# Kernel tuning notes

Measured on AMD Instinct MI355X. Metric: run time of the kernel, lower is better.

The kernel has to match this reference:

```python
import jax, jax.numpy as jnp
from jax import lax
import numpy as np

EPS = 1e-5

def _conv1x1(x, w, b=None):
    # x: [B,C,H,W], w: [O,C]
    y = jnp.einsum('oc,bchw->bohw', w, x)
    if b is not None:
        y = y + b[:, None, None]
    return y

def _bn(x, g, b, m, v):
    scale = g / jnp.sqrt(v + EPS)
    return (x - m[:, None, None]) * scale[:, None, None] + b[:, None, None]

def _conv_bn_silu(x, w, g, b, m, v):
    return jax.nn.silu(_bn(_conv1x1(x, w), g, b, m, v))

def _maxpool(x, k):
    p = k // 2
    return lax.reduce_window(x, -jnp.inf, lax.max, (1, 1, k, k), (1, 1, 1, 1),
                             ((0, 0), (0, 0), (p, p), (p, p)))

def _avgpool(x, k):
    # torch AvgPool2d default count_include_pad=True -> divide by k*k
    p = k // 2
    s = lax.reduce_window(x, 0.0, lax.add, (1, 1, k, k), (1, 1, 1, 1),
                          ((0, 0), (0, 0), (p, p), (p, p)))
    return s / float(k * k)

def setup_inputs() -> dict:
    key = jax.random.key(0)
    ks = jax.random.split(key, 18)
    f32 = jnp.float32
    B, C1, H, W = 8, 512, 64, 64
    c_ = C1 // 2          # 256
    C = c_ * 7            # 1792
    Cq = C // 8           # 224
    C2 = 512
    rn = lambda i, sh, s: jax.random.normal(ks[i], sh, dtype=f32) * s
    return {
        'x': rn(0, (B, C1, H, W), 1.0),
        'cv1_w': rn(1, (c_, C1), 0.05),
        'cv1_g': jax.random.uniform(ks[2], (c_,), dtype=f32),
        'cv1_b': rn(3, (c_,), 0.05),
        'cv1_m': jnp.zeros((c_,), f32),
        'cv1_v': jnp.ones((c_,), f32),
        'q_w': rn(4, (Cq, C), 0.02),
        'q_b': rn(5, (Cq,), 0.02),
        'k_w': rn(6, (Cq, C), 0.02),
        'k_b': rn(7, (Cq,), 0.02),
        'v_w': rn(8, (C, C), 0.02),
        'v_b': rn(9, (C,), 0.02),
        'gamma': rn(10, (1,), 0.5),
        'cv2_w': rn(11, (C2, C), 0.02),
        'cv2_g': jax.random.uniform(ks[12], (C2,), dtype=f32),
        'cv2_b': rn(13, (C2,), 0.05),
        'cv2_m': jnp.zeros((C2,), f32),
        'cv2_v': jnp.ones((C2,), f32),
    }

def _criss_cross(cat, q_w, q_b, k_w, k_b, v_w, v_b, gamma):
    B, C, H, W = cat.shape
    q = _conv1x1(cat, q_w, q_b)   # [B,Cq,H,W]
    k = _conv1x1(cat, k_w, k_b)
    v = _conv1x1(cat, v_w, v_b)   # [B,C,H,W]
    # column (H-axis) energies with -inf diagonal, row (W-axis) energies
    eH = jnp.einsum('bchw,bcgw->bhwg', q, k)        # [B,H,W,H]
    diag = jnp.eye(H, dtype=bool)[:, None, :]       # mask where h == g
    eH = jnp.where(diag, -jnp.inf, eH)
    eW = jnp.einsum('bchw,bchv->bhwv', q, k)        # [B,H,W,W]
    att = jax.nn.softmax(jnp.concatenate([eH, eW], axis=-1), axis=-1)
    attH, attW = att[..., :H], att[..., H:]
    outH = jnp.einsum('bcgw,bhwg->bchw', v, attH)
    outW = jnp.einsum('bchv,bhwv->bchw', v, attW)
    return gamma[0] * (outH + outW) + cat

def reference(x, cv1_w, cv1_g, cv1_b, cv1_m, cv1_v,
              q_w, q_b, k_w, k_b, v_w, v_b, gamma,
              cv2_w, cv2_g, cv2_b, cv2_m, cv2_v):
    x1 = _conv_bn_silu(x, cv1_w, cv1_g, cv1_b, cv1_m, cv1_v)   # [B,256,H,W]
    y1 = _maxpool(x1, 5)
    y2 = _maxpool(y1, 5)
    y3 = _maxpool(y2, 5)
    a1 = _avgpool(x1, 13)
    a2 = _avgpool(x1, 9)
    a3 = _avgpool(x1, 5)
    cat = jnp.concatenate([x1, y1, y2, y3, a1, a2, a3], axis=1)  # [B,1792,H,W]
    att = _criss_cross(cat, q_w, q_b, k_w, k_b, v_w, v_b, gamma)
    return _conv_bn_silu(att, cv2_w, cv2_g, cv2_b, cv2_m, cv2_v)
```

## Files before the change

kernel.cpp:

```cpp
#include <hip/hip_runtime.h>


typedef short bf16x8 __attribute__((ext_vector_type(8)));
typedef float f32x4  __attribute__((ext_vector_type(4)));

#define DEV __device__ __forceinline__

DEV float bf2f(unsigned short u) {
    unsigned int i = ((unsigned int)u) << 16;
    float f; __builtin_memcpy(&f, &i, 4); return f;
}
DEV unsigned short f2bf(float f) {
    unsigned int i; __builtin_memcpy(&i, &f, 4);
    unsigned int r = i + 0x7FFFu + ((i >> 16) & 1u);
    return (unsigned short)(r >> 16);
}
DEV float fsilu(float v) { return v / (1.f + __expf(-v)); }

#define GLL(gsrc, ldst)                                                        \
    __builtin_amdgcn_global_load_lds(                                          \
        (const __attribute__((address_space(1))) unsigned int*)(gsrc),         \
        (__attribute__((address_space(3))) unsigned int*)(ldst), 16, 0, 0)

#define MFMA(a, b, c) __builtin_amdgcn_mfma_f32_16x16x32_bf16((a), (b), (c), 0, 0, 0)

#define SBAR do {                                                              \
    __builtin_amdgcn_sched_barrier(0);                                         \
    __builtin_amdgcn_s_barrier();                                              \
    __builtin_amdgcn_sched_barrier(0); } while (0)
#define LGKM0 do {                                                             \
    asm volatile("s_waitcnt lgkmcnt(0)" ::: "memory");                         \
    __builtin_amdgcn_sched_barrier(0); } while (0)
#define VMC(n) do {                                                            \
    asm volatile("s_waitcnt vmcnt(" #n ")" ::: "memory");                      \
    __builtin_amdgcn_sched_barrier(0); } while (0)

template <int EPI, bool DUAL>
DEV void gemm_core(
    unsigned short (&Ash)[2][2][8192], unsigned short (&Bsh)[2][2][8192],
    int bx, int by,
    const unsigned short* __restrict__ A, const unsigned short* __restrict__ B,
    const unsigned short* __restrict__ A2, const unsigned short* __restrict__ B2,
    int lda, int ldb, int K1, int K2,
    void* __restrict__ outp, int ldo,
    const float* __restrict__ p0, const float* __restrict__ p1)
{
    const int tid = threadIdx.x, lane = tid & 63, wave = tid >> 6;
    const int wm = wave >> 2, wn = wave & 3;
    const long tile_m = (long)bx * 256;
    const long tile_n = (long)by * 256;
    const int r0 = tid >> 2;
    const int ke0 = ((tid & 3) * 8) ^ (16 * ((r0 >> 3) & 1));
    const unsigned short* As0 = A + (tile_m + r0) * (long)lda + ke0;
    const unsigned short* As1 = A + (tile_m + r0 + 128) * (long)lda + ke0;
    const unsigned short* Bs0 = B + (tile_n + r0) * (long)ldb + ke0;
    const unsigned short* Bs1 = B + (tile_n + r0 + 128) * (long)ldb + ke0;
    const unsigned short* Cs0 = DUAL ? A2 + (tile_m + r0) * (long)lda + ke0 : As0;
    const unsigned short* Cs1 = DUAL ? A2 + (tile_m + r0 + 128) * (long)lda + ke0 : As1;
    const unsigned short* Ds0 = DUAL ? B2 + (tile_n + r0) * (long)ldb + ke0 : Bs0;
    const unsigned short* Ds1 = DUAL ? B2 + (tile_n + r0 + 128) * (long)ldb + ke0 : Bs1;
    const int dst0 = wave * 512;
    const int dst1 = 4096 + wave * 512;
    const int arow = lane & 15;
    const int kgs = ((lane >> 4) << 3) ^ (16 * ((arow >> 3) & 1));
    f32x4 acc[8][4] = {};
    bf16x8 a[8], b[4];
    const int nt1 = K1 >> 6;
    const int nt = nt1 + (DUAL ? (K2 >> 6) : 0);

#define PA0(t) ((DUAL && (t) >= nt1) ? Cs0 + (long)((t) - nt1) * 64 : As0 + (long)(t) * 64)
#define PA1(t) ((DUAL && (t) >= nt1) ? Cs1 + (long)((t) - nt1) * 64 : As1 + (long)(t) * 64)
#define PB0(t) ((DUAL && (t) >= nt1) ? Ds0 + (long)((t) - nt1) * 64 : Bs0 + (long)(t) * 64)
#define PB1(t) ((DUAL && (t) >= nt1) ? Ds1 + (long)((t) - nt1) * 64 : Bs1 + (long)(t) * 64)
#define STGA(db, kh, t) do {                                                   \
    GLL(PA0(t) + (kh) * 32, &Ash[db][kh][dst0]);                               \
    GLL(PA1(t) + (kh) * 32, &Ash[db][kh][dst1]); } while (0)
#define STGB(db, kh, t) do {                                                   \
    GLL(PB0(t) + (kh) * 32, &Bsh[db][kh][dst0]);                               \
    GLL(PB1(t) + (kh) * 32, &Bsh[db][kh][dst1]); } while (0)
#define LDA8(db, ks) do { _Pragma("unroll")                                    \
    for (int m = 0; m < 8; ++m)                                                \
        a[m] = *(const bf16x8*)&Ash[db][ks][(wm * 128 + m * 16 + arow) * 32 + kgs]; \
    } while (0)
#define LDB1(db, ks, n, slot)                                                  \
    b[slot] = *(const bf16x8*)&Bsh[db][ks][(wn * 64 + (n) * 16 + arow) * 32 + kgs]
#define MMA2(lo) do {                                                          \
    __builtin_amdgcn_s_setprio(1);                                             \
    _Pragma("unroll")                                                          \
    for (int m = 0; m < 8; ++m) {                                              \
        acc[m][lo]     = MFMA(a[m], b[lo],     acc[m][lo]);                    \
        acc[m][lo + 1] = MFMA(a[m], b[lo + 1], acc[m][lo + 1]);                \
    }                                                                          \
    __builtin_amdgcn_s_setprio(0); } while (0)

    STGA(0, 0, 0); STGB(0, 0, 0);
    STGA(0, 1, 0); STGB(0, 1, 0);
    {
        const int t1p = (1 < nt) ? 1 : 0;
        STGA(1, 0, t1p); STGB(1, 0, t1p);
    }
    VMC(4);
    SBAR;

    for (int kt = 0; kt < nt; ++kt) {
        const int db = kt & 1, sb = db ^ 1;
        const int t1c = (kt + 1 < nt) ? kt + 1 : nt - 1;
        const int t2c = (kt + 2 < nt) ? kt + 2 : nt - 1;
        LDA8(db, 0);
        LDB1(db, 0, 0, 0); LDB1(db, 0, 1, 1);
        STGA(sb, 1, t1c);
        LGKM0;
        MMA2(0);
        SBAR;
        LDB1(db, 0, 2, 2); LDB1(db, 0, 3, 3);
        STGB(sb, 1, t1c);
        LGKM0;
        MMA2(2);
        SBAR;
        LDA8(db, 1);
        LDB1(db, 1, 0, 0); LDB1(db, 1, 1, 1);
        STGA(db, 0, t2c);
        LGKM0;
        MMA2(0);
        SBAR;
        LDB1(db, 1, 2, 2); LDB1(db, 1, 3, 3);
        STGB(db, 0, t2c);
        LGKM0;
        MMA2(2);
        VMC(4);
        SBAR;
    }
    VMC(0);

    const int rbase = (lane >> 4) << 2;
#pragma unroll
    for (int n = 0; n < 4; ++n) {
        const int gcol = (int)tile_n + wn * 64 + n * 16 + arow;
        const float s0 = p0[gcol];
        const float s1 = (EPI != 1) ? p1[gcol] : 0.f;
#pragma unroll
        for (int m = 0; m < 8; ++m) {
            const long grow0 = tile_m + wm * 128 + m * 16 + rbase;
            if (EPI == 4) {
                const long bb = grow0 >> 12, pix = grow0 & 4095;
                float4 o4;
#pragma unroll
                for (int r = 0; r < 4; ++r) {
                    float v = acc[m][n][r] * s0 + s1;
                    ((float*)&o4)[r] = fsilu(v);
                }
                *(float4*)&((float*)outp)[((bb * 512 + gcol)) * 4096 + pix] = o4;
            } else {
#pragma unroll
                for (int r = 0; r < 4; ++r) {
                    float v = acc[m][n][r];
                    if (EPI != 1) { v = v * s0 + s1; v = fsilu(v); }
                    else          { v += s0; }
                    ((unsigned short*)outp)[(grow0 + r) * ldo + gcol] = f2bf(v);
                }
            }
        }
    }
#undef PA0
#undef PA1
#undef PB0
#undef PB1
#undef STGA
#undef STGB
#undef LDA8
#undef LDB1
#undef MMA2
}

template <int EPI, bool DUAL>
__global__ __launch_bounds__(512, 2) void gemm_pair(
    const unsigned short* __restrict__ A, const unsigned short* __restrict__ B,
    const unsigned short* __restrict__ A2, const unsigned short* __restrict__ B2,
    int lda, int ldb, int K1, int K2,
    void* __restrict__ outp, int ldo,
    const float* __restrict__ p0, const float* __restrict__ p1)
{
    __shared__ __align__(16) unsigned short Ash[2][2][8192];
    __shared__ __align__(16) unsigned short Bsh[2][2][8192];
    const int bid = blockIdx.x;
    const int xcd = bid & 7, idx = bid >> 3;
    const int m = xcd + 8 * (idx >> 1);
    const int n = idx & 1;
    gemm_core<EPI, DUAL>(Ash, Bsh, m, n, A, B, A2, B2, lda, ldb, K1, K2,
                         outp, ldo, p0, p1);
}

__global__ __launch_bounds__(512, 2) void gemm_wcv1(
    const unsigned short* __restrict__ wc2, const unsigned short* __restrict__ wvT,
    unsigned short* __restrict__ w2g, const float* __restrict__ zeros,
    const unsigned short* __restrict__ xT, const unsigned short* __restrict__ wb1,
    unsigned short* __restrict__ catT,
    const float* __restrict__ sc1, const float* __restrict__ sh1)
{
    __shared__ __align__(16) unsigned short Ash[2][2][8192];
    __shared__ __align__(16) unsigned short Bsh[2][2][8192];
    const int bid = blockIdx.x;
    if (bid < 14) {
        const int bx = bid / 7, by = bid % 7;
        gemm_core<1, false>(Ash, Bsh, bx, by, wc2, wvT, wc2, wvT,
                            1792, 1792, 1792, 0, w2g, 1792, zeros, nullptr);
    } else {
        const int bx = bid - 14;
        gemm_core<0, false>(Ash, Bsh, bx, 0, xT, wb1, xT, wb1,
                            512, 512, 512, 0, catT, 1792, sc1, sh1);
    }
}

__global__ __launch_bounds__(256) void prep_all(
    const float* __restrict__ x, unsigned short* __restrict__ xT,
    const float* __restrict__ v_w, unsigned short* __restrict__ wvT,
    const float* __restrict__ cv1_w, const float* __restrict__ cv1_g,
    const float* __restrict__ cv1_b, const float* __restrict__ cv1_m,
    const float* __restrict__ cv1_v,
    const float* __restrict__ q_w, const float* __restrict__ q_b,
    const float* __restrict__ k_w, const float* __restrict__ k_b,
    const float* __restrict__ cv2_w,
    unsigned short* __restrict__ wb1, unsigned short* __restrict__ wqk,
    unsigned short* __restrict__ wc2,
    float* __restrict__ sc1, float* __restrict__ sh1,
    float* __restrict__ qkb, float* __restrict__ zeros,
    const float* __restrict__ cv2_g, const float* __restrict__ cv2_b,
    const float* __restrict__ cv2_m, const float* __restrict__ cv2_v,
    const float* __restrict__ v_b, const float* __restrict__ gamma,
    float* __restrict__ sc2, float* __restrict__ sh2)
{
    const int bid = blockIdx.x, tid = threadIdx.x;
    __shared__ __align__(16) float tile[64][65];
    if (bid < 4096) {
        int nt = bid & 63, ct = (bid >> 6) & 7, b = bid >> 9;
        int n0 = nt * 64, c0 = ct * 64;
#pragma unroll
        for (int it = 0; it < 16; ++it) {
            int idx = tid + it * 256;
            int r = idx >> 6, cc = idx & 63;
            tile[r][cc] = x[((long)(b * 512 + c0 + r)) * 4096 + n0 + cc];
        }
        __syncthreads();
#pragma unroll
        for (int it = 0; it < 16; ++it) {
            int idx = tid + it * 256;
            int r = idx >> 6, cc = idx & 63;
            xT[((long)(b * 4096 + n0 + r)) * 512 + c0 + cc] = f2bf(tile[cc][r]);
        }
    } else if (bid < 4880) {
        int id = bid - 4096;
        int tx = id % 28, ty = id / 28;
#pragma unroll
        for (int it = 0; it < 16; ++it) {
            int idx = tid + it * 256;
            int r = idx >> 6, cc = idx & 63;
            tile[r][cc] = v_w[((long)(ty * 64 + r)) * 1792 + tx * 64 + cc];
        }
        __syncthreads();
#pragma unroll
        for (int it = 0; it < 16; ++it) {
            int idx = tid + it * 256;
            int r = idx >> 6, cc = idx & 63;
            wvT[((long)(tx * 64 + r)) * 1792 + ty * 64 + cc] = f2bf(tile[cc][r]);
        }
    } else if (bid < 5904) {
        for (int i = (bid - 4880) * 256 + tid; i < 917504; i += 1024 * 256) {
            wc2[i] = f2bf(cv2_w[i]);
            int row = i / 1792;
            int col = i - row * 1792;
            float qv = (row < 224) ? q_w[i]
                       : (row < 448) ? k_w[(row - 224) * 1792 + col] : 0.f;
            wqk[i] = f2bf(qv);
            if (i < 131072) wb1[i] = f2bf(cv1_w[i]);
            if (i < 1792) zeros[i] = 0.f;
            if (i < 512) qkb[i] = (i < 224) ? q_b[i] : (i < 448 ? k_b[i - 224] : 0.f);
            if (i < 256) {
                float sc = cv1_g[i] * rsqrtf(cv1_v[i] + 1e-5f);
                sc1[i] = sc; sh1[i] = cv1_b[i] - cv1_m[i] * sc;
            }
        }
    } else {
        const int i = bid - 5904;
        float* red = &tile[0][0];
        float s = 0.f;
        for (int k = tid; k < 1792; k += 256) s += cv2_w[i * 1792 + k] * v_b[k];
        red[tid] = s;
        __syncthreads();
#pragma unroll
        for (int off = 128; off > 0; off >>= 1) {
            if (tid < off) red[tid] += red[tid + off];
            __syncthreads();
        }
        if (tid == 0) {
            float sc = cv2_g[i] * rsqrtf(cv2_v[i] + 1e-5f);
            sc2[i] = sc;
            sh2[i] = cv2_b[i] - cv2_m[i] * sc + sc * gamma[0] * red[0];
        }
    }
}

template <int I>
DEV void pool_h_body(const unsigned short* x1s, unsigned short* pool,
                     int c, int w0, long obase)
{
    constexpr int R = 2 * (I + 1);
    constexpr int K = 2 * R + 1;
    unsigned short* qm = pool + (long)I * 32768 * 256;
    unsigned short* qs = pool + (long)(I + 3) * 32768 * 256;
    float pre[32];
    {
        float run = -1e30f;
        int ph = (w0 + 2 * R - (K - 1)) % K;
#pragma unroll
        for (int t = 0; t < 32 + K - 1; ++t) {
            int p = w0 + R - (K - 1) + t;
            if (ph == 0) run = -1e30f;
            float v = ((unsigned)p < 64u) ? bf2f(x1s[p * 256 + c]) : -1e30f;
            run = fmaxf(run, v);
            if (t >= K - 1) pre[t - (K - 1)] = run;
            ph = (ph + 1 == K) ? 0 : ph + 1;
        }
    }
    {
        float run = -1e30f;
        int ph = (w0 + 31 + (K - 1)) % K;
#pragma unroll
        for (int t = 0; t < 32 + K - 1; ++t) {
            int s = w0 + 31 - R + (K - 1) - t;
            if (ph == K - 1) run = -1e30f;
            float v = ((unsigned)s < 64u) ? bf2f(x1s[s * 256 + c]) : -1e30f;
            run = fmaxf(run, v);
            if (t >= K - 1) {
                int w = s + R;
                qm[obase + (long)w * 16384] =
                    f2bf(fmaxf(run, pre[31 + (K - 1) - t]));
            }
            ph = (ph == 0) ? K - 1 : ph - 1;
        }
    }
    {
        float s = 0.f;
        int lo0 = (w0 - R >= 0) ? w0 - R : 0;
        int hi0 = (w0 + R <= 63) ? w0 + R : 63;
        for (int d = lo0; d <= hi0; ++d) s += bf2f(x1s[d * 256 + c]);
        for (int ww = 0; ww < 32; ++ww) {
            int w = w0 + ww;
            qs[obase + (long)w * 16384] = f2bf(s);
            if (w + 1 + R <= 63) s += bf2f(x1s[(w + 1 + R) * 256 + c]);
            if (w - R >= 0)      s -= bf2f(x1s[(w - R) * 256 + c]);
        }
    }
}

__global__ __launch_bounds__(512) void pool_h_all(
    const unsigned short* __restrict__ catT, unsigned short* __restrict__ pool)
{
    const int b = blockIdx.x >> 6, h = blockIdx.x & 63;
    __shared__ __align__(16) unsigned short x1s[64 * 256];
    const int tid = threadIdx.x, lane = tid & 63, wave = tid >> 6;
    const long nb = (long)b * 4096 + h * 64;
#pragma unroll
    for (int j = 0; j < 4; ++j) {
        int chunk = j * 8 + wave;
        int o = chunk * 1024 + lane * 16;
        int e = o >> 1, w = e >> 8, c = e & 255;
        GLL(catT + (nb + w) * 1792 + c, (char*)x1s + chunk * 1024);
    }
    __syncthreads();
    const int c = tid & 255, wg = tid >> 8;
    const int w0 = wg * 32;
    const long obase = ((long)b * 4096 + h) * 256 + c;
    pool_h_body<0>(x1s, pool, c, w0, obase);
    pool_h_body<1>(x1s, pool, c, w0, obase);
    pool_h_body<2>(x1s, pool, c, w0, obase);
}

template <int I>
DEV void pool_v_body(const unsigned short* mslab, const unsigned short* sslab,
                     unsigned short* catT, int c, int h0, long dbase)
{
    constexpr int R = 2 * (I + 1);
    constexpr int K = 2 * R + 1;
    constexpr float SCL = (I == 0) ? (1.f / 25.f)
                        : (I == 1) ? (1.f / 81.f) : (1.f / 169.f);
    constexpr int MAXD = 256 * (I + 1);
    constexpr int SUMD = 1536 - 256 * I;
    float pre[32];
    {
        float run = -1e30f;
        int ph = (h0 + 2 * R - (K - 1)) % K;
#pragma unroll
        for (int t = 0; t < 32 + K - 1; ++t) {
            int p = h0 + R - (K - 1) + t;
            if (ph == 0) run = -1e30f;
            float v = ((unsigned)p < 64u) ? bf2f(mslab[p * 128 + c]) : -1e30f;
            run = fmaxf(run, v);
            if (t >= K - 1) pre[t - (K - 1)] = run;
            ph = (ph + 1 == K) ? 0 : ph + 1;
        }
    }
    {
        float run = -1e30f;
        int ph = (h0 + 31 + (K - 1)) % K;
#pragma unroll
        for (int t = 0; t < 32 + K - 1; ++t) {
            int s = h0 + 31 - R + (K - 1) - t;
            if (ph == K - 1) run = -1e30f;
            float v = ((unsigned)s < 64u) ? bf2f(mslab[s * 128 + c]) : -1e30f;
            run = fmaxf(run, v);
            if (t >= K - 1) {
                int h = s + R;
                catT[dbase + MAXD + (long)h * (64 * 1792)] =
                    f2bf(fmaxf(run, pre[31 + (K - 1) - t]));
            }
            ph = (ph == 0) ? K - 1 : ph - 1;
        }
    }
    {
        float s = 0.f;
        int lo0 = (h0 - R >= 0) ? h0 - R : 0;
        int hi0 = (h0 + R <= 63) ? h0 + R : 63;
        for (int d = lo0; d <= hi0; ++d) s += bf2f(sslab[d * 128 + c]);
        for (int hh = 0; hh < 32; ++hh) {
            int h = h0 + hh;
            catT[dbase + SUMD + (long)h * (64 * 1792)] = f2bf(s * SCL);
            if (h + 1 + R <= 63) s += bf2f(sslab[(h + 1 + R) * 128 + c]);
            if (h - R >= 0)      s -= bf2f(sslab[(h - R) * 128 + c]);
        }
    }
}

__global__ __launch_bounds__(256) void pool_v_all(
    const unsigned short* __restrict__ pool, unsigned short* __restrict__ catT)
{
    const int s6 = blockIdx.y;
    const int bid = blockIdx.x;
    const int chh = bid & 1, w = (bid >> 1) & 63, b = bid >> 7;
    const int c0 = chh * 128;
    __shared__ __align__(16) unsigned short mslab[64 * 128];
    __shared__ __align__(16) unsigned short sslab[64 * 128];
    const int tid = threadIdx.x, lane = tid & 63, wave = tid >> 6;
    const long sbase = ((long)b * 4096 + (long)w * 64) * 256 + c0;
    const unsigned short* msrc = pool + (long)s6 * 32768 * 256 + sbase;
    const unsigned short* ssrc = pool + (long)(s6 + 3) * 32768 * 256 + sbase;
#pragma unroll
    for (int j = 0; j < 4; ++j) {
        int o = j * 4096 + wave * 1024 + lane * 16;
        int hh = o >> 8, ce = (o & 255) >> 1;
        GLL(msrc + hh * 256 + ce, (char*)mslab + (j * 4096 + wave * 1024));
        GLL(ssrc + hh * 256 + ce, (char*)sslab + (j * 4096 + wave * 1024));
    }
    __syncthreads();
    const int c = tid & 127, hg = tid >> 7;
    const int h0 = hg * 32;
    const long dbase = ((long)b * 4096 + w) * 1792 + c0 + c;
    if (s6 == 0)      pool_v_body<0>(mslab, sslab, catT, c, h0, dbase);
    else if (s6 == 1) pool_v_body<1>(mslab, sslab, catT, c, h0, dbase);
    else              pool_v_body<2>(mslab, sslab, catT, c, h0, dbase);
}

__global__ __launch_bounds__(256) void scores_h(
    const unsigned short* __restrict__ qk, float* __restrict__ attHlog)
{
    const int b = blockIdx.x >> 6, w = blockIdx.x & 63;
    __shared__ __align__(16) unsigned short Qs[64 * 232];
    __shared__ __align__(16) unsigned short Ks[64 * 232];
    const int tid = threadIdx.x, lane = tid & 63, wave = tid >> 6;
#pragma unroll
    for (int j = 0; j < 14; ++j) {
        int idx = tid + j * 256;
        int s = idx >= 1792;
        int id2 = idx - s * 1792;
        int row = id2 / 28, cb = id2 - row * 28;
        bf16x8 v = *(const bf16x8*)(qk + ((long)b * 4096 + row * 64 + w) * 512 +
                                    s * 224 + cb * 8);
        *(bf16x8*)((s ? Ks : Qs) + row * 232 + cb * 8) = v;
    }
    __syncthreads();
    const int m0 = wave * 16, arow = lane & 15, kc = (lane >> 4) << 3;
    f32x4 acc[4] = {};
#pragma unroll
    for (int ks = 0; ks < 7; ++ks) {
        bf16x8 af = *(const bf16x8*)(Qs + (m0 + arow) * 232 + ks * 32 + kc);
#pragma unroll
        for (int nf = 0; nf < 4; ++nf) {
            bf16x8 bv = *(const bf16x8*)(Ks + (nf * 16 + arow) * 232 + ks * 32 + kc);
            acc[nf] = MFMA(af, bv, acc[nf]);
        }
    }
    const int rb = (lane >> 4) << 2;
#pragma unroll
    for (int nf = 0; nf < 4; ++nf) {
        int g = nf * 16 + arow;
#pragma unroll
        for (int r = 0; r < 4; ++r) {
            int h = m0 + rb + r;
            float v = acc[nf][r];
            if (g == h) v = -1e30f;
            attHlog[((long)(b * 64 + h) * 64 + w) * 64 + g] = v;
        }
    }
}

__global__ __launch_bounds__(256) void scores_w_softmax(
    const unsigned short* __restrict__ qk, const float* __restrict__ attHlog,
    unsigned short* __restrict__ att)
{
    const int b = blockIdx.x >> 6, h = blockIdx.x & 63;
    __shared__ __align__(16) unsigned short Qs[64 * 232];
    __shared__ __align__(16) unsigned short Ks[64 * 232];
    __shared__ float ews[64 * 65];
    const int tid = threadIdx.x, lane = tid & 63, wave = tid >> 6;
    const long nbase = (long)b * 4096 + h * 64;
#pragma unroll
    for (int j = 0; j < 14; ++j) {
        int idx = tid + j * 256;
        int s = idx >= 1792;
        int id2 = idx - s * 1792;
        int row = id2 / 28, cb = id2 - row * 28;
        bf16x8 v = *(const bf16x8*)(qk + (nbase + row) * 512 + s * 224 + cb * 8);
        *(bf16x8*)((s ? Ks : Qs) + row * 232 + cb * 8) = v;
    }
    __syncthreads();
    const int m0 = wave * 16, arow = lane & 15, kc = (lane >> 4) << 3;
    f32x4 acc[4] = {};
#pragma unroll
    for (int ks = 0; ks < 7; ++ks) {
        bf16x8 af = *(const bf16x8*)(Qs + (m0 + arow) * 232 + ks * 32 + kc);
#pragma unroll
        for (int nf = 0; nf < 4; ++nf) {
            bf16x8 bv = *(const bf16x8*)(Ks + (nf * 16 + arow) * 232 + ks * 32 + kc);
            acc[nf] = MFMA(af, bv, acc[nf]);
        }
    }
    const int rb = (lane >> 4) << 2;
#pragma unroll
    for (int nf = 0; nf < 4; ++nf)
#pragma unroll
        for (int r = 0; r < 4; ++r)
            ews[(m0 + rb + r) * 65 + nf * 16 + arow] = acc[nf][r];
    __syncthreads();
    const int wl = tid >> 2, p = tid & 3;
    float eh[16], ew[16];
    const float* hrow = attHlog + ((long)(b * 64 + h) * 64 + wl) * 64 + p * 16;
#pragma unroll
    for (int j = 0; j < 16; ++j) eh[j] = hrow[j];
#pragma unroll
    for (int j = 0; j < 16; ++j) ew[j] = ews[wl * 65 + p * 16 + j];
    float mx = -1e30f;
#pragma unroll
    for (int j = 0; j < 16; ++j) { mx = fmaxf(mx, eh[j]); mx = fmaxf(mx, ew[j]); }
    mx = fmaxf(mx, __shfl_xor(mx, 1));
    mx = fmaxf(mx, __shfl_xor(mx, 2));
    float sm = 0.f;
#pragma unroll
    for (int j = 0; j < 16; ++j) {
        eh[j] = __expf(eh[j] - mx); sm += eh[j];
        ew[j] = __expf(ew[j] - mx); sm += ew[j];
    }
    sm += __shfl_xor(sm, 1);
    sm += __shfl_xor(sm, 2);
    float inv = 1.f / sm;
    unsigned short* orow = att + ((long)(b * 64 + h) * 64 + wl) * 128;
#pragma unroll
    for (int j = 0; j < 16; ++j) orow[p * 16 + j] = f2bf(eh[j] * inv);
#pragma unroll
    for (int j = 0; j < 16; ++j) orow[64 + p * 16 + j] = f2bf(ew[j] * inv);
}

template <int MODE>
__global__ __launch_bounds__(256) void apply_att(
    const unsigned short* __restrict__ att, const unsigned short* __restrict__ vsrc,
    unsigned short* __restrict__ mixed, const float* __restrict__ gamma)
{
    const int ch = blockIdx.x & 3;
    const int i  = (blockIdx.x >> 2) & 63;
    const int b  = blockIdx.x >> 8;
    const int c0 = ch * 448;
    __shared__ __align__(16) unsigned short As[64 * 72];
    __shared__ __align__(16) unsigned short Vs[64 * 448];
    const int tid = threadIdx.x, lane = tid & 63, wave = tid >> 6;
#pragma unroll
    for (int j = 0; j < 2; ++j) {
        int idx = tid + j * 256;
        int hh = idx >> 3, cb = idx & 7;
        long pos = (MODE == 0) ? ((long)(b * 64 + hh) * 64 + i)
                               : ((long)(b * 64 + i) * 64 + hh);
        bf16x8 v = *(const bf16x8*)(att + pos * 128 + MODE * 64 + cb * 8);
        *(bf16x8*)(As + hh * 72 + cb * 8) = v;
    }
#pragma unroll
    for (int j = 0; j < 14; ++j) {
        int idx = tid + j * 256;
        int g = idx / 56, cb = idx - g * 56;
        long n = (MODE == 0) ? ((long)b * 4096 + g * 64 + i)
                             : ((long)b * 4096 + i * 64 + g);
        bf16x8 v = *(const bf16x8*)(vsrc + n * 1792 + c0 + cb * 8);
        int sw = (g >> 3) & 7;
        *(bf16x8*)(Vs + g * 448 + ((cb ^ sw) << 3)) = v;
    }
    __syncthreads();
    const int arow = lane & 15, kc8 = (lane >> 4) << 3;
    const int rb = (lane >> 4) << 2;
    f32x4 acc[4][7] = {};
#pragma unroll
    for (int ks = 0; ks < 2; ++ks) {
        const int k0 = ks * 32;
        bf16x8 af[4];
#pragma unroll
        for (int m = 0; m < 4; ++m)
            af[m] = *(const bf16x8*)(As + (m * 16 + arow) * 72 + k0 + kc8);
        const int g0 = k0 + kc8;
        const int sw = (g0 >> 3) & 7;
#pragma unroll
        for (int nf = 0; nf < 7; ++nf) {
            int cl = wave * 112 + nf * 16 + arow;
            int cb = cl >> 3, clo = cl & 7;
            const unsigned short* pp = Vs + g0 * 448 + ((cb ^ sw) << 3) + clo;
            bf16x8 bv;
#pragma unroll
            for (int j = 0; j < 8; ++j) bv[j] = (short)pp[j * 448];
#pragma unroll
            for (int m = 0; m < 4; ++m)
                acc[m][nf] = MFMA(af[m], bv, acc[m][nf]);
        }
    }
    const float gam = gamma[0];
#pragma unroll
    for (int nf = 0; nf < 7; ++nf) {
        const int c = c0 + wave * 112 + nf * 16 + arow;
#pragma unroll
        for (int m = 0; m < 4; ++m) {
#pragma unroll
            for (int r = 0; r < 4; ++r) {
                const int rl = m * 16 + rb + r;
                long n = (MODE == 0) ? ((long)b * 4096 + rl * 64 + i)
                                     : ((long)b * 4096 + i * 64 + rl);
                long idx2 = n * 1792 + c;
                if (MODE == 0) {
                    mixed[idx2] = f2bf(acc[m][nf][r]);
                } else {
                    float pv = bf2f(mixed[idx2]);
                    mixed[idx2] = f2bf(gam * (acc[m][nf][r] + pv));
                }
            }
        }
    }
}

extern "C" void kernel_launch(void* const* d_in, const int* in_sizes, int n_in,
                              void* d_out, int out_size, void* d_ws, size_t ws_size,
                              hipStream_t stream)
{
    const float* x     = (const float*)d_in[0];
    const float* cv1_w = (const float*)d_in[1];
    const float* cv1_g = (const float*)d_in[2];
    const float* cv1_b = (const float*)d_in[3];
    const float* cv1_m = (const float*)d_in[4];
    const float* cv1_v = (const float*)d_in[5];
    const float* q_w   = (const float*)d_in[6];
    const float* q_b   = (const float*)d_in[7];
    const float* k_w   = (const float*)d_in[8];
    const float* k_b   = (const float*)d_in[9];
    const float* v_w   = (const float*)d_in[10];
    const float* v_b   = (const float*)d_in[11];
    const float* gamma = (const float*)d_in[12];
    const float* cv2_w = (const float*)d_in[13];
    const float* cv2_g = (const float*)d_in[14];
    const float* cv2_b = (const float*)d_in[15];
    const float* cv2_m = (const float*)d_in[16];
    const float* cv2_v = (const float*)d_in[17];

    char* ws = (char*)d_ws;
    unsigned short* wb1  = (unsigned short*)(ws + 0);
    unsigned short* wqk  = (unsigned short*)(ws + 262144);
    unsigned short* wc2  = (unsigned short*)(ws + 2097152);
    unsigned short* w2g  = (unsigned short*)(ws + 3932160);
    float* sc1           = (float*)(ws + 5767168);
    float* sh1           = (float*)(ws + 5775360);
    float* sc2           = (float*)(ws + 5783552);
    float* sh2           = (float*)(ws + 5791744);
    float* qkb           = (float*)(ws + 5799936);
    float* zeros         = (float*)(ws + 5808128);
    unsigned short* catT = (unsigned short*)(ws + 6291456);
    const long C_OFF = 123731968;
    unsigned short* xT    = (unsigned short*)(ws + C_OFF);
    unsigned short* wvT   = (unsigned short*)(ws + C_OFF + 33554432);
    unsigned short* poolb = (unsigned short*)(ws + C_OFF);
    unsigned short* mixed = (unsigned short*)(ws + C_OFF);
    unsigned short* qk    = (unsigned short*)d_out;
    float* attHlog        = (float*)((char*)d_out + 33554432);
    unsigned short* attb  = (unsigned short*)((char*)d_out + 41943040);

    prep_all<<<6416, 256, 0, stream>>>(
        x, xT, v_w, wvT,
        cv1_w, cv1_g, cv1_b, cv1_m, cv1_v, q_w, q_b, k_w, k_b, cv2_w,
        wb1, wqk, wc2, sc1, sh1, qkb, zeros,
        cv2_g, cv2_b, cv2_m, cv2_v, v_b, gamma, sc2, sh2);

    gemm_wcv1<<<142, 512, 0, stream>>>(wc2, wvT, w2g, zeros,
                                       xT, wb1, catT, sc1, sh1);

    pool_h_all<<<512, 512, 0, stream>>>(catT, poolb);
    pool_v_all<<<dim3(1024, 3), 256, 0, stream>>>(poolb, catT);

    gemm_pair<1, false><<<256, 512, 0, stream>>>(
        catT, wqk, catT, wqk, 1792, 1792, 1792, 0, qk, 512, qkb, nullptr);

    scores_h<<<512, 256, 0, stream>>>(qk, attHlog);
    scores_w_softmax<<<512, 256, 0, stream>>>(qk, attHlog, attb);

    apply_att<0><<<2048, 256, 0, stream>>>(attb, catT, mixed, gamma);
    apply_att<1><<<2048, 256, 0, stream>>>(attb, catT, mixed, gamma);

    gemm_pair<4, true><<<256, 512, 0, stream>>>(
        mixed, w2g, catT, wc2, 1792, 1792, 1792, 1792, d_out, 0, sc2, sh2);
}
```

Baseline: 513.1 us.

## Shrink GEMM K-tile to 32 with simpler double-buffered pipeline

The GEMM core moves from a K=64 tile split into two 32-wide halves with four interleaved stage/compute phases to a K=32 tile with a plain two-buffer prefetch-by-two loop. LDS use per block is halved (64KB to 32KB), and each iteration does one sync-load-compute round instead of four. The cost is twice as many loop iterations and barriers per unit of K, and less fine-grained overlap of global-to-LDS loads with MFMA work. The VMC(4) wait count is kept, and it now covers a single four-load STG batch.

```diff
diff --git a/kernel.cpp b/kernel.cpp
--- a/kernel.cpp
+++ b/kernel.cpp
@@ -37,7 +37,7 @@
 
 template <int EPI, bool DUAL>
 DEV void gemm_core(
-    unsigned short (&Ash)[2][2][8192], unsigned short (&Bsh)[2][2][8192],
+    unsigned short (&Ash)[2][8192], unsigned short (&Bsh)[2][8192],
     int bx, int by,
     const unsigned short* __restrict__ A, const unsigned short* __restrict__ B,
     const unsigned short* __restrict__ A2, const unsigned short* __restrict__ B2,
@@ -65,25 +65,24 @@
     const int kgs = ((lane >> 4) << 3) ^ (16 * ((arow >> 3) & 1));
     f32x4 acc[8][4] = {};
     bf16x8 a[8], b[4];
-    const int nt1 = K1 >> 6;
-    const int nt = nt1 + (DUAL ? (K2 >> 6) : 0);
-
-#define PA0(t) ((DUAL && (t) >= nt1) ? Cs0 + (long)((t) - nt1) * 64 : As0 + (long)(t) * 64)
-#define PA1(t) ((DUAL && (t) >= nt1) ? Cs1 + (long)((t) - nt1) * 64 : As1 + (long)(t) * 64)
-#define PB0(t) ((DUAL && (t) >= nt1) ? Ds0 + (long)((t) - nt1) * 64 : Bs0 + (long)(t) * 64)
-#define PB1(t) ((DUAL && (t) >= nt1) ? Ds1 + (long)((t) - nt1) * 64 : Bs1 + (long)(t) * 64)
-#define STGA(db, kh, t) do {                                                   \
-    GLL(PA0(t) + (kh) * 32, &Ash[db][kh][dst0]);                               \
-    GLL(PA1(t) + (kh) * 32, &Ash[db][kh][dst1]); } while (0)
-#define STGB(db, kh, t) do {                                                   \
-    GLL(PB0(t) + (kh) * 32, &Bsh[db][kh][dst0]);                               \
-    GLL(PB1(t) + (kh) * 32, &Bsh[db][kh][dst1]); } while (0)
-#define LDA8(db, ks) do { _Pragma("unroll")                                    \
+    const int nt1 = K1 >> 5;
+    const int nt = nt1 + (DUAL ? (K2 >> 5) : 0);
+
+#define PA0(t) ((DUAL && (t) >= nt1) ? Cs0 + (long)((t) - nt1) * 32 : As0 + (long)(t) * 32)
+#define PA1(t) ((DUAL && (t) >= nt1) ? Cs1 + (long)((t) - nt1) * 32 : As1 + (long)(t) * 32)
+#define PB0(t) ((DUAL && (t) >= nt1) ? Ds0 + (long)((t) - nt1) * 32 : Bs0 + (long)(t) * 32)
+#define PB1(t) ((DUAL && (t) >= nt1) ? Ds1 + (long)((t) - nt1) * 32 : Bs1 + (long)(t) * 32)
+#define STG(bf, t) do {                                                        \
+    GLL(PA0(t), &Ash[bf][dst0]);                                               \
+    GLL(PA1(t), &Ash[bf][dst1]);                                               \
+    GLL(PB0(t), &Bsh[bf][dst0]);                                               \
+    GLL(PB1(t), &Bsh[bf][dst1]); } while (0)
+#define LDA8(db) do { _Pragma("unroll")                                        \
     for (int m = 0; m < 8; ++m)                                                \
-        a[m] = *(const bf16x8*)&Ash[db][ks][(wm * 128 + m * 16 + arow) * 32 + kgs]; \
+        a[m] = *(const bf16x8*)&Ash[db][(wm * 128 + m * 16 + arow) * 32 + kgs];\
     } while (0)
-#define LDB1(db, ks, n, slot)                                                  \
-    b[slot] = *(const bf16x8*)&Bsh[db][ks][(wn * 64 + (n) * 16 + arow) * 32 + kgs]
+#define LDB1(db, n, slot)                                                      \
+    b[slot] = *(const bf16x8*)&Bsh[db][(wn * 64 + (n) * 16 + arow) * 32 + kgs]
 #define MMA2(lo) do {                                                          \
     __builtin_amdgcn_s_setprio(1);                                             \
     _Pragma("unroll")                                                          \
@@ -93,39 +92,20 @@
     }                                                                          \
     __builtin_amdgcn_s_setprio(0); } while (0)
 
-    STGA(0, 0, 0); STGB(0, 0, 0);
-    STGA(0, 1, 0); STGB(0, 1, 0);
-    {
-        const int t1p = (1 < nt) ? 1 : 0;
-        STGA(1, 0, t1p); STGB(1, 0, t1p);
-    }
+    STG(0, 0);
+    STG(1, (1 < nt) ? 1 : 0);
     VMC(4);
     SBAR;
 
     for (int kt = 0; kt < nt; ++kt) {
-        const int db = kt & 1, sb = db ^ 1;
-        const int t1c = (kt + 1 < nt) ? kt + 1 : nt - 1;
+        const int db = kt & 1;
         const int t2c = (kt + 2 < nt) ? kt + 2 : nt - 1;
-        LDA8(db, 0);
-        LDB1(db, 0, 0, 0); LDB1(db, 0, 1, 1);
-        STGA(sb, 1, t1c);
+        LDA8(db);
+        LDB1(db, 0, 0); LDB1(db, 1, 1); LDB1(db, 2, 2); LDB1(db, 3, 3);
         LGKM0;
+        SBAR;
+        STG(db, t2c);
         MMA2(0);
-        SBAR;
-        LDB1(db, 0, 2, 2); LDB1(db, 0, 3, 3);
-        STGB(sb, 1, t1c);
-        LGKM0;
-        MMA2(2);
-        SBAR;
-        LDA8(db, 1);
-        LDB1(db, 1, 0, 0); LDB1(db, 1, 1, 1);
-        STGA(db, 0, t2c);
-        LGKM0;
-        MMA2(0);
-        SBAR;
-        LDB1(db, 1, 2, 2); LDB1(db, 1, 3, 3);
-        STGB(db, 0, t2c);
-        LGKM0;
         MMA2(2);
         VMC(4);
         SBAR;
@@ -165,8 +145,7 @@
 #undef PA1
 #undef PB0
 #undef PB1
-#undef STGA
-#undef STGB
+#undef STG
 #undef LDA8
 #undef LDB1
 #undef MMA2
@@ -180,8 +159,8 @@
     void* __restrict__ outp, int ldo,
     const float* __restrict__ p0, const float* __restrict__ p1)
 {
-    __shared__ __align__(16) unsigned short Ash[2][2][8192];
-    __shared__ __align__(16) unsigned short Bsh[2][2][8192];
+    __shared__ __align__(16) unsigned short Ash[2][8192];
+    __shared__ __align__(16) unsigned short Bsh[2][8192];
     const int bid = blockIdx.x;
     const int xcd = bid & 7, idx = bid >> 3;
     const int m = xcd + 8 * (idx >> 1);
@@ -197,8 +176,8 @@
     unsigned short* __restrict__ catT,
     const float* __restrict__ sc1, const float* __restrict__ sh1)
 {
-    __shared__ __align__(16) unsigned short Ash[2][2][8192];
-    __shared__ __align__(16) unsigned short Bsh[2][2][8192];
+    __shared__ __align__(16) unsigned short Ash[2][8192];
+    __shared__ __align__(16) unsigned short Bsh[2][8192];
     const int bid = blockIdx.x;
     if (bid < 14) {
         const int bx = bid / 7, by = bid % 7;
```

Result: slower. 548.9 us (+7.0%).

## Restructure GEMM LDS layout to row-halves with 64-wide K and XOR swizzle

Applied to the files above, without the earlier changes.

Changes the shared-memory staging from K-half splitting to M/N row-half splitting, with full 64-element K rows per row and an 8-way XOR swizzle. Each wave now keeps all B fragments for both K sub-steps in registers and streams A in four quarter-steps, so the wave-to-row mapping becomes interleaved (m*32 + wm*16). Prefetch ordering and the vmcnt wait depth are adjusted to match, and extra barriers are added before each MFMA phase. The aim is fewer LDS bank conflicts and better load/MFMA interleaving, at the cost of more barriers and higher register pressure.

```diff
diff --git a/kernel.cpp b/kernel.cpp
--- a/kernel.cpp
+++ b/kernel.cpp
@@ -49,85 +49,96 @@
     const int wm = wave >> 2, wn = wave & 3;
     const long tile_m = (long)bx * 256;
     const long tile_n = (long)by * 256;
-    const int r0 = tid >> 2;
-    const int ke0 = ((tid & 3) * 8) ^ (16 * ((r0 >> 3) & 1));
-    const unsigned short* As0 = A + (tile_m + r0) * (long)lda + ke0;
-    const unsigned short* As1 = A + (tile_m + r0 + 128) * (long)lda + ke0;
-    const unsigned short* Bs0 = B + (tile_n + r0) * (long)ldb + ke0;
-    const unsigned short* Bs1 = B + (tile_n + r0 + 128) * (long)ldb + ke0;
-    const unsigned short* Cs0 = DUAL ? A2 + (tile_m + r0) * (long)lda + ke0 : As0;
-    const unsigned short* Cs1 = DUAL ? A2 + (tile_m + r0 + 128) * (long)lda + ke0 : As1;
-    const unsigned short* Ds0 = DUAL ? B2 + (tile_n + r0) * (long)ldb + ke0 : Bs0;
-    const unsigned short* Ds1 = DUAL ? B2 + (tile_n + r0 + 128) * (long)ldb + ke0 : Bs1;
-    const int dst0 = wave * 512;
-    const int dst1 = 4096 + wave * 512;
+    const int rsrc = tid >> 3;
+    const int kel0 = 8 * ((tid & 7) ^ ((tid >> 3) & 7));
+    const unsigned short* pA[2] = {
+        A + (tile_m + rsrc) * (long)lda + kel0,
+        A + (tile_m + 128 + rsrc) * (long)lda + kel0 };
+    const unsigned short* pB[2] = {
+        B + (tile_n + rsrc) * (long)ldb + kel0,
+        B + (tile_n + 128 + rsrc) * (long)ldb + kel0 };
+    const unsigned short* pC[2] = {
+        DUAL ? A2 + (tile_m + rsrc) * (long)lda + kel0 : pA[0],
+        DUAL ? A2 + (tile_m + 128 + rsrc) * (long)lda + kel0 : pA[1] };
+    const unsigned short* pD[2] = {
+        DUAL ? B2 + (tile_n + rsrc) * (long)ldb + kel0 : pB[0],
+        DUAL ? B2 + (tile_n + 128 + rsrc) * (long)ldb + kel0 : pB[1] };
+    const int dstw = wave * 512;
     const int arow = lane & 15;
-    const int kgs = ((lane >> 4) << 3) ^ (16 * ((arow >> 3) & 1));
+    const int kb0 = (lane >> 4) << 3;
+    const int kxor = 8 * (arow & 7);
+    const int kk0 = kb0 ^ kxor, kk1 = kk0 ^ 32;
+    const int bhalf = wn >> 1;
+    const int brow0 = (wn & 1) * 64 + arow;
+    const int arl0 = wm * 16 + arow;
     f32x4 acc[8][4] = {};
-    bf16x8 a[8], b[4];
+    bf16x8 a[2][2], b[4][2];
     const int nt1 = K1 >> 6;
     const int nt = nt1 + (DUAL ? (K2 >> 6) : 0);
 
-#define PA0(t) ((DUAL && (t) >= nt1) ? Cs0 + (long)((t) - nt1) * 64 : As0 + (long)(t) * 64)
-#define PA1(t) ((DUAL && (t) >= nt1) ? Cs1 + (long)((t) - nt1) * 64 : As1 + (long)(t) * 64)
-#define PB0(t) ((DUAL && (t) >= nt1) ? Ds0 + (long)((t) - nt1) * 64 : Bs0 + (long)(t) * 64)
-#define PB1(t) ((DUAL && (t) >= nt1) ? Ds1 + (long)((t) - nt1) * 64 : Bs1 + (long)(t) * 64)
-#define STGA(db, kh, t) do {                                                   \
-    GLL(PA0(t) + (kh) * 32, &Ash[db][kh][dst0]);                               \
-    GLL(PA1(t) + (kh) * 32, &Ash[db][kh][dst1]); } while (0)
-#define STGB(db, kh, t) do {                                                   \
-    GLL(PB0(t) + (kh) * 32, &Bsh[db][kh][dst0]);                               \
-    GLL(PB1(t) + (kh) * 32, &Bsh[db][kh][dst1]); } while (0)
-#define LDA8(db, ks) do { _Pragma("unroll")                                    \
-    for (int m = 0; m < 8; ++m)                                                \
-        a[m] = *(const bf16x8*)&Ash[db][ks][(wm * 128 + m * 16 + arow) * 32 + kgs]; \
-    } while (0)
-#define LDB1(db, ks, n, slot)                                                  \
-    b[slot] = *(const bf16x8*)&Bsh[db][ks][(wn * 64 + (n) * 16 + arow) * 32 + kgs]
-#define MMA2(lo) do {                                                          \
+#define SRCA(h, t) (((DUAL && (t) >= nt1) ? pC[h] : pA[h]) +                   \
+                    (long)((DUAL && (t) >= nt1) ? (t) - nt1 : (t)) * 64)
+#define SRCB(h, t) (((DUAL && (t) >= nt1) ? pD[h] : pB[h]) +                   \
+                    (long)((DUAL && (t) >= nt1) ? (t) - nt1 : (t)) * 64)
+#define STG_A(buf, h, t) do {                                                  \
+    GLL(SRCA(h, t), &Ash[buf][h][dstw]);                                       \
+    GLL(SRCA(h, t) + (long)64 * lda, &Ash[buf][h][4096 + dstw]); } while (0)
+#define STG_B(buf, h, t) do {                                                  \
+    GLL(SRCB(h, t), &Bsh[buf][h][dstw]);                                       \
+    GLL(SRCB(h, t) + (long)64 * ldb, &Bsh[buf][h][4096 + dstw]); } while (0)
+#define LDB_ALL(d) do { _Pragma("unroll")                                      \
+    for (int n = 0; n < 4; ++n) {                                              \
+        b[n][0] = *(const bf16x8*)&Bsh[d][bhalf][(brow0 + n * 16) * 64 + kk0]; \
+        b[n][1] = *(const bf16x8*)&Bsh[d][bhalf][(brow0 + n * 16) * 64 + kk1]; \
+    } } while (0)
+#define LDA_Q(d, q) do { _Pragma("unroll")                                     \
+    for (int i = 0; i < 2; ++i) {                                              \
+        const int rl = ((q) & 1) * 64 + i * 32 + arl0;                         \
+        a[i][0] = *(const bf16x8*)&Ash[d][(q) >> 1][rl * 64 + kk0];            \
+        a[i][1] = *(const bf16x8*)&Ash[d][(q) >> 1][rl * 64 + kk1];            \
+    } } while (0)
+#define MMAQ(q) do {                                                           \
     __builtin_amdgcn_s_setprio(1);                                             \
     _Pragma("unroll")                                                          \
-    for (int m = 0; m < 8; ++m) {                                              \
-        acc[m][lo]     = MFMA(a[m], b[lo],     acc[m][lo]);                    \
-        acc[m][lo + 1] = MFMA(a[m], b[lo + 1], acc[m][lo + 1]);                \
-    }                                                                          \
+    for (int i = 0; i < 2; ++i) { _Pragma("unroll")                            \
+        for (int n = 0; n < 4; ++n) {                                          \
+            acc[2 * (q) + i][n] = MFMA(a[i][0], b[n][0], acc[2 * (q) + i][n]); \
+            acc[2 * (q) + i][n] = MFMA(a[i][1], b[n][1], acc[2 * (q) + i][n]); \
+        } }                                                                    \
     __builtin_amdgcn_s_setprio(0); } while (0)
 
-    STGA(0, 0, 0); STGB(0, 0, 0);
-    STGA(0, 1, 0); STGB(0, 1, 0);
+    STG_B(0, 0, 0); STG_A(0, 0, 0); STG_B(0, 1, 0); STG_A(0, 1, 0);
     {
         const int t1p = (1 < nt) ? 1 : 0;
-        STGA(1, 0, t1p); STGB(1, 0, t1p);
-    }
-    VMC(4);
+        STG_B(1, 0, t1p); STG_A(1, 0, t1p); STG_B(1, 1, t1p);
+    }
+    VMC(6);
     SBAR;
 
     for (int kt = 0; kt < nt; ++kt) {
-        const int db = kt & 1, sb = db ^ 1;
+        const int d = kt & 1;
         const int t1c = (kt + 1 < nt) ? kt + 1 : nt - 1;
         const int t2c = (kt + 2 < nt) ? kt + 2 : nt - 1;
-        LDA8(db, 0);
-        LDB1(db, 0, 0, 0); LDB1(db, 0, 1, 1);
-        STGA(sb, 1, t1c);
-        LGKM0;
-        MMA2(0);
+        LDB_ALL(d); LDA_Q(d, 0);
+        STG_A(d ^ 1, 1, t1c);
+        SBAR; LGKM0;
+        MMAQ(0);
         SBAR;
-        LDB1(db, 0, 2, 2); LDB1(db, 0, 3, 3);
-        STGB(sb, 1, t1c);
-        LGKM0;
-        MMA2(2);
+        LDA_Q(d, 1);
+        STG_B(d, 0, t2c);
+        SBAR; LGKM0;
+        MMAQ(1);
         SBAR;
-        LDA8(db, 1);
-        LDB1(db, 1, 0, 0); LDB1(db, 1, 1, 1);
-        STGA(db, 0, t2c);
-        LGKM0;
-        MMA2(0);
+        LDA_Q(d, 2);
+        STG_A(d, 0, t2c);
+        SBAR; LGKM0;
+        MMAQ(2);
         SBAR;
-        LDB1(db, 1, 2, 2); LDB1(db, 1, 3, 3);
-        STGB(db, 0, t2c);
-        LGKM0;
-        MMA2(2);
-        VMC(4);
+        LDA_Q(d, 3);
+        STG_B(d, 1, t2c);
+        SBAR; LGKM0;
+        MMAQ(3);
+        VMC(6);
         SBAR;
     }
     VMC(0);
@@ -140,7 +151,7 @@
         const float s1 = (EPI != 1) ? p1[gcol] : 0.f;
 #pragma unroll
         for (int m = 0; m < 8; ++m) {
-            const long grow0 = tile_m + wm * 128 + m * 16 + rbase;
+            const long grow0 = tile_m + m * 32 + wm * 16 + rbase;
             if (EPI == 4) {
                 const long bb = grow0 >> 12, pix = grow0 & 4095;
                 float4 o4;
@@ -161,15 +172,13 @@
             }
         }
     }
-#undef PA0
-#undef PA1
-#undef PB0
-#undef PB1
-#undef STGA
-#undef STGB
-#undef LDA8
-#undef LDB1
-#undef MMA2
+#undef SRCA
+#undef SRCB
+#undef STG_A
+#undef STG_B
+#undef LDB_ALL
+#undef LDA_Q
+#undef MMAQ
 }
 
 template <int EPI, bool DUAL>
```

After: 552.5 us. 7.7% more time.
